# Performance work log

Hardware: AMD Instinct MI355X
Metric: run time of the kernel (lower is better)

Reference implementation:

```python
import jax, jax.numpy as jnp
import numpy as np

IN_DIM = 256
QK_DIM = IN_DIM // 8


def setup_inputs() -> dict:
    key = jax.random.key(0)
    ks = jax.random.split(key, 10)
    B, C, W, H = 4, IN_DIM, 64, 64
    a = jax.random.normal(ks[0], (B, C, W, H), dtype=jnp.float32)
    b = jax.random.normal(ks[1], (B, C, W, H), dtype=jnp.float32)
    c = jax.random.uniform(ks[2], (B, 1, 2 * W, 2 * H), dtype=jnp.float32)
    scale = 0.02
    wq = jax.random.normal(ks[3], (QK_DIM, C), dtype=jnp.float32) * scale
    bq = jnp.zeros((QK_DIM,), dtype=jnp.float32)
    wk = jax.random.normal(ks[4], (QK_DIM, C), dtype=jnp.float32) * scale
    bk = jnp.zeros((QK_DIM,), dtype=jnp.float32)
    wv = jax.random.normal(ks[5], (C, C), dtype=jnp.float32) * scale
    bv = jnp.zeros((C,), dtype=jnp.float32)
    gamma = jnp.ones((1,), dtype=jnp.float32)
    return {"a": a, "b": b, "c": c, "wq": wq, "bq": bq, "wk": wk,
            "bk": bk, "wv": wv, "bv": bv, "gamma": gamma}


def reference(a, b, c, wq, bq, wk, bk, wv, bv, gamma):
    B, C, W, H = a.shape
    N = W * H
    # F.interpolate(c, scale_factor=1/down_rate, mode='nearest'): output idx i -> input idx i*down_rate
    down = c.shape[2] // W
    cd = c[:, :, ::down, ::down]                      # [B,1,W,H]
    # 1x1 convs as channel contractions
    q = jnp.einsum('bchw,oc->bohw', a, wq) + bq[None, :, None, None]
    k = jnp.einsum('bchw,oc->bohw', b, wk) + bk[None, :, None, None]
    v = jnp.einsum('bchw,oc->bohw', a, wv) + bv[None, :, None, None]
    qf = q.reshape(B, QK_DIM, N)                      # proj_query^T rows are spatial
    kf = k.reshape(B, QK_DIM, N)
    vf = v.reshape(B, C, N)
    sim = jnp.einsum('bdi,bdj->bij', qf, kf)          # [B,N,N]
    cflat = cd.reshape(B, N)
    # mask[b,i,j] = cflat[b,i] (per-query multiplicative logit scaling)
    logits = sim * cflat[:, :, None]
    attn = jax.nn.softmax(logits, axis=-1)            # [B,N,N]
    out_attn = jnp.einsum('bcj,bij->bci', vf, attn).reshape(B, C, W, H)
    out = gamma * a * cd + (1.0 - cd) * out_attn
    return out
```

## Files before the change

### kernel.cpp

```cpp
#include <hip/hip_runtime.h>

#define LOG2E 1.44269504088896340736f

typedef __attribute__((ext_vector_type(8))) short short8;
typedef __attribute__((ext_vector_type(4))) float float4v;
typedef __attribute__((ext_vector_type(2))) float float2v;
typedef __attribute__((ext_vector_type(2))) int int2v;
typedef __attribute__((ext_vector_type(4))) int int4v;

__device__ inline unsigned short f2bf(float f) {
    union { float f; unsigned u; } v; v.f = f;
    unsigned r = v.u + 0x7fffu + ((v.u >> 16) & 1u);
    return (unsigned short)(r >> 16);
}
__device__ inline float bf2f(unsigned short u) {
    union { unsigned u; float f; } v; v.u = ((unsigned)u) << 16;
    return v.f;
}
__device__ inline unsigned pk_bf16(float a, float b) {
    union { float f; unsigned u; } ua, ub; ua.f = a; ub.f = b;
    return __builtin_amdgcn_perm(ub.u + 0x8000u, ua.u + 0x8000u, 0x07060302u);
}
__device__ inline unsigned cvtpk_bf16(float a, float b) {
    unsigned r;
    asm("v_cvt_pk_bf16_f32 %0, %1, %2" : "=v"(r) : "v"(a), "v"(b));
    return r;
}

__global__ void wcvt_kernel(const float* __restrict__ wq, const float* __restrict__ wk,
                            const float* __restrict__ wv, unsigned short* __restrict__ Wbf)
{
    int idx = blockIdx.x * 256 + threadIdx.x;
    int e4  = idx * 4;
    int row = e4 >> 8, col = e4 & 255;
    const float* src = (row < 32) ? (wq + row * 256 + col)
                     : (row < 64) ? (wk + (row - 32) * 256 + col)
                                  : (wv + (row - 64) * 256 + col);
    float4v v = *(const float4v*)src;
    int2v p;
    p.x = (unsigned)f2bf(v[0]) | ((unsigned)f2bf(v[1]) << 16);
    p.y = (unsigned)f2bf(v[2]) | ((unsigned)f2bf(v[3]) << 16);
    *(int2v*)(Wbf + e4) = p;
}

__launch_bounds__(512, 2)
__global__ void proj_kernel(const float* __restrict__ a_p, const float* __restrict__ b_p,
                            const float* __restrict__ c_p,
                            const float* __restrict__ bq, const float* __restrict__ bk,
                            const float* __restrict__ bv,
                            const unsigned short* __restrict__ Wbf,
                            unsigned short* __restrict__ Qg, unsigned short* __restrict__ Kg,
                            unsigned short* __restrict__ Vg)
{
    __shared__ __align__(16) unsigned short At[64 * 266];
    __shared__ __align__(16) unsigned short Bt[64 * 266];
    __shared__ float bias[320];
    __shared__ float cdl[64];

    const int t    = threadIdx.x;
    const int blk  = blockIdx.x;
    const int b    = blk & 3;
    const int tile = blk >> 2;
    const int i0   = tile * 64;
    const int lane = t & 63;
    const int w    = t >> 6;
    const int q    = lane >> 4;
    const int n    = lane & 15;
    const int it   = w & 3;
    const int mh   = w >> 2;

    {
        const int arr = t >> 8, tt = t & 255;
        unsigned* dst = (unsigned*)(arr ? Bt : At);
        const float* base = (arr ? b_p : a_p) + (size_t)b * 256 * 4096 + i0;
#pragma unroll
        for (int r = 0; r < 8; ++r) {
            int task = r * 256 + tt;
            int cp = task >> 4, px4 = (task & 15) * 4;
            const float* s0 = base + (size_t)(2 * cp) * 4096 + px4;
            float4v r0 = *(const float4v*)s0;
            float4v r1 = *(const float4v*)(s0 + 4096);
#pragma unroll
            for (int k = 0; k < 4; ++k)
                dst[(px4 + k) * 133 + cp] = pk_bf16(r0[k], r1[k]);
        }
        if (t < 320) bias[t] = (t < 32) ? bq[t] : (t < 64) ? bk[t - 32] : bv[t - 64];
        else if (t < 384) cdl[t - 320] = c_p[b * 16384 + tile * 256 + (t - 320) * 2];
    }
    __syncthreads();

    float4v acc[10];
#pragma unroll
    for (int j = 0; j < 10; ++j) acc[j] = (float4v){0.f, 0.f, 0.f, 0.f};

#pragma unroll 2
    for (int kc = 0; kc < 8; ++kc) {
        short8 xa = *(const short8*)&At[(it * 16 + n) * 266 + kc * 32 + q * 8];
        short8 xb = xa;
        if (mh == 0)
            xb = *(const short8*)&Bt[(it * 16 + n) * 266 + kc * 32 + q * 8];
#pragma unroll
        for (int j = 0; j < 10; ++j) {
            int mt = mh * 10 + j;
            short8 wf = *(const short8*)(Wbf + (size_t)(mt * 16 + n) * 256 + kc * 32 + q * 8);
            short8 bsel = (mt == 2 || mt == 3) ? xb : xa;
            acc[j] = __builtin_amdgcn_mfma_f32_16x16x32_bf16(wf, bsel, acc[j], 0, 0, 0);
        }
    }
    __syncthreads();

    unsigned short* QKst = At;
    unsigned short* Vst  = Bt;
    {
        const float cdq = cdl[it * 16 + n] * LOG2E;
#pragma unroll
        for (int j = 0; j < 10; ++j) {
            int mt = mh * 10 + j;
            float4v bv4 = *(const float4v*)&bias[mt * 16 + q * 4];
            float v0 = acc[j][0] + bv4[0], v1 = acc[j][1] + bv4[1];
            float v2 = acc[j][2] + bv4[2], v3 = acc[j][3] + bv4[3];
            if (mt < 2) {
                v0 *= cdq; v1 *= cdq; v2 *= cdq; v3 *= cdq;
                int2v pk; pk.x = (int)pk_bf16(v0, v1); pk.y = (int)pk_bf16(v2, v3);
                *(int2v*)&QKst[(it * 16 + n) * 72 + mt * 16 + q * 4] = pk;
            } else if (mt < 4) {
                int2v pk; pk.x = (int)pk_bf16(v0, v1); pk.y = (int)pk_bf16(v2, v3);
                *(int2v*)&QKst[(it * 16 + n) * 72 + mt * 16 + q * 4] = pk;
            } else {
                int p = ((n >> 2) * 8) + ((it & 1) * 4) + (n & 3);
                int cbase = mt * 16 - 64 + q * 4;
                int jb = it >> 1;
                Vst[((jb * 256) + cbase + 0) * 32 + p] = f2bf(v0);
                Vst[((jb * 256) + cbase + 1) * 32 + p] = f2bf(v1);
                Vst[((jb * 256) + cbase + 2) * 32 + p] = f2bf(v2);
                Vst[((jb * 256) + cbase + 3) * 32 + p] = f2bf(v3);
            }
        }
    }
    __syncthreads();

    {
        int i = t >> 3, h8 = t & 7;
        int4v v = *(const int4v*)&QKst[i * 72 + h8 * 8];
        unsigned short* dstp = (h8 < 4)
            ? Qg + (size_t)(b * 4096 + i0 + i) * 32 + h8 * 8
            : Kg + (size_t)(b * 4096 + i0 + i) * 32 + (h8 - 4) * 8;
        *(int4v*)dstp = v;
    }
    {
#pragma unroll
        for (int k = 0; k < 4; ++k) {
            int flat = k * 512 + t;
            int4v v = *(const int4v*)&Vst[flat * 8];
            int jb = flat >> 10;
            *(int4v*)(Vg + (size_t)(b * 128 + tile * 2 + jb) * 8192 + (flat & 1023) * 8) = v;
        }
    }
}

__launch_bounds__(256, 3)
__global__ void attn_kernel(const unsigned short* __restrict__ Qg,
                            const unsigned short* __restrict__ Kg,
                            const unsigned short* __restrict__ Vg,
                            unsigned short* __restrict__ Opart, float* __restrict__ lsum)
{
    __shared__ __align__(16) unsigned short Pbuf[2][4][64 * 8];

    const int t    = threadIdx.x;
    const int blk  = blockIdx.x;
    const int b    = blk & 3;
    const int rt   = (blk >> 2) & 63;
    const int s    = blk >> 8;
    const int ni   = (s == 2) ? 32 : 48;
    const int lidx = (s << 8) | (rt << 2) | b;
    const int i0   = rt * 64;
    const int lane = t & 63;
    const int w    = t >> 6;
    const int q    = lane >> 4;
    const int n    = lane & 15;

    short8 qf = *(const short8*)(Qg + (size_t)(b * 4096 + i0 + w * 16 + n) * 32 + q * 8);

    float4v acc[4][4];
#pragma unroll
    for (int ig = 0; ig < 4; ++ig)
#pragma unroll
        for (int ct = 0; ct < 4; ++ct) acc[ig][ct] = (float4v){0.f, 0.f, 0.f, 0.f};
    float lsc = 0.f;

    const float4v m16v = (float4v){-16.f, -16.f, -16.f, -16.f};

    const unsigned short* kb = Kg + (size_t)(b * 4096 + s * 1536 + n) * 32 + q * 8;
    const unsigned short* vb = Vg + ((size_t)((b * 128 + s * 48) * 256 + w * 64 + n)) * 32 + q * 8;

    short8 vf[4];
#pragma unroll
    for (int ct = 0; ct < 4; ++ct)
        vf[ct] = *(const short8*)(vb + ct * 512);
    short8 kf0 = *(const short8*)(kb);
    short8 kf1 = *(const short8*)(kb + 512);

    {
        float4v s0 = __builtin_amdgcn_mfma_f32_16x16x32_bf16(kf0, qf, m16v, 0, 0, 0);
        float4v s1 = __builtin_amdgcn_mfma_f32_16x16x32_bf16(kf1, qf, m16v, 0, 0, 0);
        kf0 = *(const short8*)(kb + 1024);
        kf1 = *(const short8*)(kb + 1536);
        float p0 = __builtin_amdgcn_exp2f(s0[0]), p1 = __builtin_amdgcn_exp2f(s0[1]);
        float p2 = __builtin_amdgcn_exp2f(s0[2]), p3 = __builtin_amdgcn_exp2f(s0[3]);
        float p4 = __builtin_amdgcn_exp2f(s1[0]), p5 = __builtin_amdgcn_exp2f(s1[1]);
        float p6 = __builtin_amdgcn_exp2f(s1[2]), p7 = __builtin_amdgcn_exp2f(s1[3]);
        lsc += ((p0 + p1) + (p2 + p3)) + ((p4 + p5) + (p6 + p7));
        union { short8 s8; unsigned u[4]; } pf_;
        pf_.u[0] = cvtpk_bf16(p0, p1);
        pf_.u[1] = cvtpk_bf16(p2, p3);
        pf_.u[2] = cvtpk_bf16(p4, p5);
        pf_.u[3] = cvtpk_bf16(p6, p7);
        *(short8*)&Pbuf[0][w][lane * 8] = pf_.s8;
    }
    __syncthreads();
    short8 pfc[4];
#pragma unroll
    for (int ig = 0; ig < 4; ++ig)
        pfc[ig] = *(const short8*)&Pbuf[0][ig][lane * 8];

    kb += 2048;
    vb += 8192;

#pragma unroll 1
    for (int it = 0; it < ni - 1; ++it) {
        float4v s0 = __builtin_amdgcn_mfma_f32_16x16x32_bf16(kf0, qf, m16v, 0, 0, 0);
        float4v s1 = __builtin_amdgcn_mfma_f32_16x16x32_bf16(kf1, qf, m16v, 0, 0, 0);
        kf0 = *(const short8*)(kb);
        kf1 = *(const short8*)(kb + 512);

        __builtin_amdgcn_s_setprio(1);
#pragma unroll
        for (int ig = 0; ig < 4; ++ig)
#pragma unroll
            for (int ct = 0; ct < 4; ++ct)
                acc[ig][ct] = __builtin_amdgcn_mfma_f32_16x16x32_bf16(pfc[ig], vf[ct], acc[ig][ct], 0, 0, 0);
        __builtin_amdgcn_s_setprio(0);

#pragma unroll
        for (int ct = 0; ct < 4; ++ct)
            vf[ct] = *(const short8*)(vb + ct * 512);

        {
            float p0 = __builtin_amdgcn_exp2f(s0[0]), p1 = __builtin_amdgcn_exp2f(s0[1]);
            float p2 = __builtin_amdgcn_exp2f(s0[2]), p3 = __builtin_amdgcn_exp2f(s0[3]);
            float p4 = __builtin_amdgcn_exp2f(s1[0]), p5 = __builtin_amdgcn_exp2f(s1[1]);
            float p6 = __builtin_amdgcn_exp2f(s1[2]), p7 = __builtin_amdgcn_exp2f(s1[3]);
            lsc += ((p0 + p1) + (p2 + p3)) + ((p4 + p5) + (p6 + p7));
            union { short8 s8; unsigned u[4]; } pf_;
            pf_.u[0] = cvtpk_bf16(p0, p1);
            pf_.u[1] = cvtpk_bf16(p2, p3);
            pf_.u[2] = cvtpk_bf16(p4, p5);
            pf_.u[3] = cvtpk_bf16(p6, p7);
            *(short8*)&Pbuf[(it + 1) & 1][w][lane * 8] = pf_.s8;
        }
        __syncthreads();
#pragma unroll
        for (int ig = 0; ig < 4; ++ig)
            pfc[ig] = *(const short8*)&Pbuf[(it + 1) & 1][ig][lane * 8];

        kb += 1024;
        vb += 8192;
    }

#pragma unroll
    for (int ig = 0; ig < 4; ++ig)
#pragma unroll
        for (int ct = 0; ct < 4; ++ct)
            acc[ig][ct] = __builtin_amdgcn_mfma_f32_16x16x32_bf16(pfc[ig], vf[ct], acc[ig][ct], 0, 0, 0);

    const size_t obase = (size_t)lidx * 16384;
#pragma unroll
    for (int ig = 0; ig < 4; ++ig)
#pragma unroll
        for (int ct = 0; ct < 4; ++ct) {
            int c = w * 64 + ct * 16 + n;
            int i = ig * 16 + q * 4;
            int2v pk;
            pk.x = (int)pk_bf16(acc[ig][ct][0], acc[ig][ct][1]);
            pk.y = (int)pk_bf16(acc[ig][ct][2], acc[ig][ct][3]);
            *(int2v*)(Opart + obase + (size_t)c * 64 + i) = pk;
        }
    {
        float v = lsc;
        v += __shfl_xor(v, 16, 64);
        v += __shfl_xor(v, 32, 64);
        if (lane < 16)
            lsum[(size_t)lidx * 64 + w * 16 + lane] = v;
    }
}

__launch_bounds__(256, 4)
__global__ void combine_kernel(const float* __restrict__ a_p, const float* __restrict__ c_p,
                               const float* __restrict__ gamma_p,
                               const unsigned short* __restrict__ Opart,
                               const float* __restrict__ lsum, float* __restrict__ out)
{
    __shared__ float invL[64];
    __shared__ float cdl[64];

    const int t   = threadIdx.x;
    const int blk = blockIdx.x;
    const int b   = blk & 3;
    const int rt  = (blk >> 2) & 63;
    const int cs  = blk >> 8;
    const int i0  = rt * 64;

    if (t < 64) {
        float L = 0.f;
#pragma unroll
        for (int s = 0; s < 3; ++s)
            L += lsum[(size_t)((s << 8) | (rt << 2) | b) * 64 + t];
        invL[t] = 1.0f / L;
        cdl[t] = c_p[b * 16384 + rt * 256 + 2 * t];
    }
    __syncthreads();

    const float gam = gamma_p[0];
    const int c  = cs * 32 + (t >> 3);
    const int e8 = (t & 7) * 8;
    float o[8];
#pragma unroll
    for (int r = 0; r < 8; ++r) o[r] = 0.f;
#pragma unroll
    for (int s = 0; s < 3; ++s) {
        int idx = (s << 8) | (rt << 2) | b;
        int4v pv = *(const int4v*)(Opart + (size_t)idx * 16384 + (size_t)c * 64 + e8);
#pragma unroll
        for (int h = 0; h < 4; ++h) {
            unsigned u = (unsigned)pv[h];
            o[2 * h]     += bf2f((unsigned short)(u & 0xffffu));
            o[2 * h + 1] += bf2f((unsigned short)(u >> 16));
        }
    }
    size_t gi = (size_t)(b * 256 + c) * 4096 + i0 + e8;
    float4v a0 = *(const float4v*)(a_p + gi);
    float4v a1 = *(const float4v*)(a_p + gi + 4);
    float4v ov0, ov1;
#pragma unroll
    for (int r = 0; r < 4; ++r) {
        float cd0 = cdl[e8 + r],     l0 = invL[e8 + r];
        float cd1 = cdl[e8 + 4 + r], l1 = invL[e8 + 4 + r];
        ov0[r] = gam * a0[r] * cd0 + (1.0f - cd0) * (o[r] * l0);
        ov1[r] = gam * a1[r] * cd1 + (1.0f - cd1) * (o[4 + r] * l1);
    }
    *(float4v*)(out + gi) = ov0;
    *(float4v*)(out + gi + 4) = ov1;
}

extern "C" void kernel_launch(void* const* d_in, const int* in_sizes, int n_in,
                              void* d_out, int out_size, void* d_ws, size_t ws_size,
                              hipStream_t stream)
{
    const float* a_p   = (const float*)d_in[0];
    const float* b_p   = (const float*)d_in[1];
    const float* c_p   = (const float*)d_in[2];
    const float* wq    = (const float*)d_in[3];
    const float* bq    = (const float*)d_in[4];
    const float* wk    = (const float*)d_in[5];
    const float* bk    = (const float*)d_in[6];
    const float* wv    = (const float*)d_in[7];
    const float* bv    = (const float*)d_in[8];
    const float* gamma = (const float*)d_in[9];
    float* out = (float*)d_out;

    unsigned short* Qg    = (unsigned short*)d_ws;
    unsigned short* Kg    = Qg + (size_t)4 * 4096 * 32;
    unsigned short* Vg    = Kg + (size_t)4 * 4096 * 32;
    unsigned short* Wbf   = Vg + (size_t)4 * 256 * 4096;
    unsigned short* Opart = Wbf + (size_t)320 * 256;
    float*          lsum  = (float*)(Opart + (size_t)768 * 16384);

    wcvt_kernel<<<80, 256, 0, stream>>>(wq, wk, wv, Wbf);
    proj_kernel<<<256, 512, 0, stream>>>(a_p, b_p, c_p, bq, bk, bv, Wbf, Qg, Kg, Vg);
    attn_kernel<<<768, 256, 0, stream>>>(Qg, Kg, Vg, Opart, lsum);
    combine_kernel<<<2048, 256, 0, stream>>>(a_p, c_p, gamma, Opart, lsum, out);
}
```

Baseline: 175.3 us.

## Keep P in registers per wave and split V columns instead of sharing via LDS

Each wave now keeps its own 16 query rows' P fragment in registers and accumulates across all 256 value channels, instead of exchanging P tiles through a double-buffered LDS array with a __syncthreads every iteration. This removes the per-iteration block barrier and LDS traffic. In exchange each wave loads all 16 V fragments per step, four times the V global/L2 read traffic, with register ping-pong prefetching between two V buffers.

Measured after the change: 263.2 us. 1.5x slower.

```diff
diff --git a/kernel.cpp b/kernel.cpp
--- a/kernel.cpp
+++ b/kernel.cpp
@@ -164,8 +164,6 @@
                             const unsigned short* __restrict__ Vg,
                             unsigned short* __restrict__ Opart, float* __restrict__ lsum)
 {
-    __shared__ __align__(16) unsigned short Pbuf[2][4][64 * 8];
-
     const int t    = threadIdx.x;
     const int blk  = blockIdx.x;
     const int b    = blk & 3;
@@ -181,25 +179,20 @@
 
     short8 qf = *(const short8*)(Qg + (size_t)(b * 4096 + i0 + w * 16 + n) * 32 + q * 8);
 
-    float4v acc[4][4];
-#pragma unroll
-    for (int ig = 0; ig < 4; ++ig)
-#pragma unroll
-        for (int ct = 0; ct < 4; ++ct) acc[ig][ct] = (float4v){0.f, 0.f, 0.f, 0.f};
+    float4v acc[16];
+#pragma unroll
+    for (int ct = 0; ct < 16; ++ct) acc[ct] = (float4v){0.f, 0.f, 0.f, 0.f};
     float lsc = 0.f;
 
     const float4v m16v = (float4v){-16.f, -16.f, -16.f, -16.f};
 
     const unsigned short* kb = Kg + (size_t)(b * 4096 + s * 1536 + n) * 32 + q * 8;
-    const unsigned short* vb = Vg + ((size_t)((b * 128 + s * 48) * 256 + w * 64 + n)) * 32 + q * 8;
-
-    short8 vf[4];
-#pragma unroll
-    for (int ct = 0; ct < 4; ++ct)
-        vf[ct] = *(const short8*)(vb + ct * 512);
+    const unsigned short* vb = Vg + ((size_t)((b * 128 + s * 48) * 256 + n)) * 32 + q * 8;
+
     short8 kf0 = *(const short8*)(kb);
     short8 kf1 = *(const short8*)(kb + 512);
 
+    short8 pfc;
     {
         float4v s0 = __builtin_amdgcn_mfma_f32_16x16x32_bf16(kf0, qf, m16v, 0, 0, 0);
         float4v s1 = __builtin_amdgcn_mfma_f32_16x16x32_bf16(kf1, qf, m16v, 0, 0, 0);
@@ -215,16 +208,13 @@
         pf_.u[1] = cvtpk_bf16(p2, p3);
         pf_.u[2] = cvtpk_bf16(p4, p5);
         pf_.u[3] = cvtpk_bf16(p6, p7);
-        *(short8*)&Pbuf[0][w][lane * 8] = pf_.s8;
-    }
-    __syncthreads();
-    short8 pfc[4];
-#pragma unroll
-    for (int ig = 0; ig < 4; ++ig)
-        pfc[ig] = *(const short8*)&Pbuf[0][ig][lane * 8];
-
+        pfc = pf_.s8;
+    }
+    short8 vfP[4], vfQ[4];
+#pragma unroll
+    for (int k = 0; k < 4; ++k)
+        vfP[k] = *(const short8*)(vb + k * 512);
     kb += 2048;
-    vb += 8192;
 
 #pragma unroll 1
     for (int it = 0; it < ni - 1; ++it) {
@@ -235,15 +225,26 @@
 
         __builtin_amdgcn_s_setprio(1);
 #pragma unroll
-        for (int ig = 0; ig < 4; ++ig)
-#pragma unroll
-            for (int ct = 0; ct < 4; ++ct)
-                acc[ig][ct] = __builtin_amdgcn_mfma_f32_16x16x32_bf16(pfc[ig], vf[ct], acc[ig][ct], 0, 0, 0);
+        for (int k = 0; k < 4; ++k) vfQ[k] = *(const short8*)(vb + (4 + k) * 512);
+#pragma unroll
+        for (int k = 0; k < 4; ++k)
+            acc[k] = __builtin_amdgcn_mfma_f32_16x16x32_bf16(pfc, vfP[k], acc[k], 0, 0, 0);
+#pragma unroll
+        for (int k = 0; k < 4; ++k) vfP[k] = *(const short8*)(vb + (8 + k) * 512);
+#pragma unroll
+        for (int k = 0; k < 4; ++k)
+            acc[4 + k] = __builtin_amdgcn_mfma_f32_16x16x32_bf16(pfc, vfQ[k], acc[4 + k], 0, 0, 0);
+#pragma unroll
+        for (int k = 0; k < 4; ++k) vfQ[k] = *(const short8*)(vb + (12 + k) * 512);
+#pragma unroll
+        for (int k = 0; k < 4; ++k)
+            acc[8 + k] = __builtin_amdgcn_mfma_f32_16x16x32_bf16(pfc, vfP[k], acc[8 + k], 0, 0, 0);
+#pragma unroll
+        for (int k = 0; k < 4; ++k) vfP[k] = *(const short8*)(vb + 8192 + k * 512);
+#pragma unroll
+        for (int k = 0; k < 4; ++k)
+            acc[12 + k] = __builtin_amdgcn_mfma_f32_16x16x32_bf16(pfc, vfQ[k], acc[12 + k], 0, 0, 0);
         __builtin_amdgcn_s_setprio(0);
-
-#pragma unroll
-        for (int ct = 0; ct < 4; ++ct)
-            vf[ct] = *(const short8*)(vb + ct * 512);
 
         {
             float p0 = __builtin_amdgcn_exp2f(s0[0]), p1 = __builtin_amdgcn_exp2f(s0[1]);
@@ -256,35 +257,42 @@
             pf_.u[1] = cvtpk_bf16(p2, p3);
             pf_.u[2] = cvtpk_bf16(p4, p5);
             pf_.u[3] = cvtpk_bf16(p6, p7);
-            *(short8*)&Pbuf[(it + 1) & 1][w][lane * 8] = pf_.s8;
-        }
-        __syncthreads();
-#pragma unroll
-        for (int ig = 0; ig < 4; ++ig)
-            pfc[ig] = *(const short8*)&Pbuf[(it + 1) & 1][ig][lane * 8];
+            pfc = pf_.s8;
+        }
 
         kb += 1024;
         vb += 8192;
     }
 
 #pragma unroll
-    for (int ig = 0; ig < 4; ++ig)
-#pragma unroll
-        for (int ct = 0; ct < 4; ++ct)
-            acc[ig][ct] = __builtin_amdgcn_mfma_f32_16x16x32_bf16(pfc[ig], vf[ct], acc[ig][ct], 0, 0, 0);
+    for (int k = 0; k < 4; ++k) vfQ[k] = *(const short8*)(vb + (4 + k) * 512);
+#pragma unroll
+    for (int k = 0; k < 4; ++k)
+        acc[k] = __builtin_amdgcn_mfma_f32_16x16x32_bf16(pfc, vfP[k], acc[k], 0, 0, 0);
+#pragma unroll
+    for (int k = 0; k < 4; ++k) vfP[k] = *(const short8*)(vb + (8 + k) * 512);
+#pragma unroll
+    for (int k = 0; k < 4; ++k)
+        acc[4 + k] = __builtin_amdgcn_mfma_f32_16x16x32_bf16(pfc, vfQ[k], acc[4 + k], 0, 0, 0);
+#pragma unroll
+    for (int k = 0; k < 4; ++k) vfQ[k] = *(const short8*)(vb + (12 + k) * 512);
+#pragma unroll
+    for (int k = 0; k < 4; ++k)
+        acc[8 + k] = __builtin_amdgcn_mfma_f32_16x16x32_bf16(pfc, vfP[k], acc[8 + k], 0, 0, 0);
+#pragma unroll
+    for (int k = 0; k < 4; ++k)
+        acc[12 + k] = __builtin_amdgcn_mfma_f32_16x16x32_bf16(pfc, vfQ[k], acc[12 + k], 0, 0, 0);
 
     const size_t obase = (size_t)lidx * 16384;
 #pragma unroll
-    for (int ig = 0; ig < 4; ++ig)
-#pragma unroll
-        for (int ct = 0; ct < 4; ++ct) {
-            int c = w * 64 + ct * 16 + n;
-            int i = ig * 16 + q * 4;
-            int2v pk;
-            pk.x = (int)pk_bf16(acc[ig][ct][0], acc[ig][ct][1]);
-            pk.y = (int)pk_bf16(acc[ig][ct][2], acc[ig][ct][3]);
-            *(int2v*)(Opart + obase + (size_t)c * 64 + i) = pk;
-        }
+    for (int ct = 0; ct < 16; ++ct) {
+        int c = ct * 16 + n;
+        int i = w * 16 + q * 4;
+        int2v pk;
+        pk.x = (int)pk_bf16(acc[ct][0], acc[ct][1]);
+        pk.y = (int)pk_bf16(acc[ct][2], acc[ct][3]);
+        *(int2v*)(Opart + obase + (size_t)c * 64 + i) = pk;
+    }
     {
         float v = lsc;
         v += __shfl_xor(v, 16, 64);
```

## Process two key tiles per loop iteration to halve barriers in attention

Applied to the files above, without the earlier changes.

Each main-loop iteration now handles two 32-key chunks. It computes four QK MFMAs, writes two P fragments to a doubled LDS buffer, and runs 32 PV MFMAs, so half as many iterations and __syncthreads are needed. V fragments are loaded inside the loop right before use instead of being prefetched one iteration ahead. This trades barrier and loop overhead for higher register pressure and V load latency that is now exposed.

Result: slower. 179.3 us (+2.3%).

```diff
diff --git a/kernel.cpp b/kernel.cpp
--- a/kernel.cpp
+++ b/kernel.cpp
@@ -164,14 +164,14 @@
                             const unsigned short* __restrict__ Vg,
                             unsigned short* __restrict__ Opart, float* __restrict__ lsum)
 {
-    __shared__ __align__(16) unsigned short Pbuf[2][4][64 * 8];
+    __shared__ __align__(16) unsigned short Pbuf[2][4][2][64 * 8];
 
     const int t    = threadIdx.x;
     const int blk  = blockIdx.x;
     const int b    = blk & 3;
     const int rt   = (blk >> 2) & 63;
     const int s    = blk >> 8;
-    const int ni   = (s == 2) ? 32 : 48;
+    const int nr   = (s == 2) ? 16 : 24;
     const int lidx = (s << 8) | (rt << 2) | b;
     const int i0   = rt * 64;
     const int lane = t & 63;
@@ -193,85 +193,127 @@
     const unsigned short* kb = Kg + (size_t)(b * 4096 + s * 1536 + n) * 32 + q * 8;
     const unsigned short* vb = Vg + ((size_t)((b * 128 + s * 48) * 256 + w * 64 + n)) * 32 + q * 8;
 
-    short8 vf[4];
-#pragma unroll
-    for (int ct = 0; ct < 4; ++ct)
-        vf[ct] = *(const short8*)(vb + ct * 512);
-    short8 kf0 = *(const short8*)(kb);
-    short8 kf1 = *(const short8*)(kb + 512);
-
-    {
-        float4v s0 = __builtin_amdgcn_mfma_f32_16x16x32_bf16(kf0, qf, m16v, 0, 0, 0);
-        float4v s1 = __builtin_amdgcn_mfma_f32_16x16x32_bf16(kf1, qf, m16v, 0, 0, 0);
-        kf0 = *(const short8*)(kb + 1024);
-        kf1 = *(const short8*)(kb + 1536);
-        float p0 = __builtin_amdgcn_exp2f(s0[0]), p1 = __builtin_amdgcn_exp2f(s0[1]);
-        float p2 = __builtin_amdgcn_exp2f(s0[2]), p3 = __builtin_amdgcn_exp2f(s0[3]);
-        float p4 = __builtin_amdgcn_exp2f(s1[0]), p5 = __builtin_amdgcn_exp2f(s1[1]);
-        float p6 = __builtin_amdgcn_exp2f(s1[2]), p7 = __builtin_amdgcn_exp2f(s1[3]);
-        lsc += ((p0 + p1) + (p2 + p3)) + ((p4 + p5) + (p6 + p7));
-        union { short8 s8; unsigned u[4]; } pf_;
-        pf_.u[0] = cvtpk_bf16(p0, p1);
-        pf_.u[1] = cvtpk_bf16(p2, p3);
-        pf_.u[2] = cvtpk_bf16(p4, p5);
-        pf_.u[3] = cvtpk_bf16(p6, p7);
-        *(short8*)&Pbuf[0][w][lane * 8] = pf_.s8;
+    short8 kfs[4];
+#pragma unroll
+    for (int k = 0; k < 4; ++k) kfs[k] = *(const short8*)(kb + k * 512);
+
+    {
+        float4v sA0 = __builtin_amdgcn_mfma_f32_16x16x32_bf16(kfs[0], qf, m16v, 0, 0, 0);
+        float4v sA1 = __builtin_amdgcn_mfma_f32_16x16x32_bf16(kfs[1], qf, m16v, 0, 0, 0);
+        float4v sB0 = __builtin_amdgcn_mfma_f32_16x16x32_bf16(kfs[2], qf, m16v, 0, 0, 0);
+        float4v sB1 = __builtin_amdgcn_mfma_f32_16x16x32_bf16(kfs[3], qf, m16v, 0, 0, 0);
+#pragma unroll
+        for (int k = 0; k < 4; ++k) kfs[k] = *(const short8*)(kb + 2048 + k * 512);
+        float a0 = __builtin_amdgcn_exp2f(sA0[0]), a1 = __builtin_amdgcn_exp2f(sA0[1]);
+        float a2 = __builtin_amdgcn_exp2f(sA0[2]), a3 = __builtin_amdgcn_exp2f(sA0[3]);
+        float a4 = __builtin_amdgcn_exp2f(sA1[0]), a5 = __builtin_amdgcn_exp2f(sA1[1]);
+        float a6 = __builtin_amdgcn_exp2f(sA1[2]), a7 = __builtin_amdgcn_exp2f(sA1[3]);
+        float b0 = __builtin_amdgcn_exp2f(sB0[0]), b1 = __builtin_amdgcn_exp2f(sB0[1]);
+        float b2 = __builtin_amdgcn_exp2f(sB0[2]), b3 = __builtin_amdgcn_exp2f(sB0[3]);
+        float b4 = __builtin_amdgcn_exp2f(sB1[0]), b5 = __builtin_amdgcn_exp2f(sB1[1]);
+        float b6 = __builtin_amdgcn_exp2f(sB1[2]), b7 = __builtin_amdgcn_exp2f(sB1[3]);
+        lsc += ((a0 + a1) + (a2 + a3)) + ((a4 + a5) + (a6 + a7))
+             + ((b0 + b1) + (b2 + b3)) + ((b4 + b5) + (b6 + b7));
+        union { short8 s8; unsigned u[4]; } pA_, pB_;
+        pA_.u[0] = cvtpk_bf16(a0, a1); pA_.u[1] = cvtpk_bf16(a2, a3);
+        pA_.u[2] = cvtpk_bf16(a4, a5); pA_.u[3] = cvtpk_bf16(a6, a7);
+        pB_.u[0] = cvtpk_bf16(b0, b1); pB_.u[1] = cvtpk_bf16(b2, b3);
+        pB_.u[2] = cvtpk_bf16(b4, b5); pB_.u[3] = cvtpk_bf16(b6, b7);
+        *(short8*)&Pbuf[0][w][0][lane * 8] = pA_.s8;
+        *(short8*)&Pbuf[0][w][1][lane * 8] = pB_.s8;
     }
     __syncthreads();
-    short8 pfc[4];
-#pragma unroll
-    for (int ig = 0; ig < 4; ++ig)
-        pfc[ig] = *(const short8*)&Pbuf[0][ig][lane * 8];
-
-    kb += 2048;
-    vb += 8192;
+    short8 pfc[4][2];
+#pragma unroll
+    for (int ig = 0; ig < 4; ++ig) {
+        pfc[ig][0] = *(const short8*)&Pbuf[0][ig][0][lane * 8];
+        pfc[ig][1] = *(const short8*)&Pbuf[0][ig][1][lane * 8];
+    }
+    kb += 4096;
 
 #pragma unroll 1
-    for (int it = 0; it < ni - 1; ++it) {
-        float4v s0 = __builtin_amdgcn_mfma_f32_16x16x32_bf16(kf0, qf, m16v, 0, 0, 0);
-        float4v s1 = __builtin_amdgcn_mfma_f32_16x16x32_bf16(kf1, qf, m16v, 0, 0, 0);
-        kf0 = *(const short8*)(kb);
-        kf1 = *(const short8*)(kb + 512);
+    for (int r = 0; r < nr - 1; ++r) {
+        float4v sA0 = __builtin_amdgcn_mfma_f32_16x16x32_bf16(kfs[0], qf, m16v, 0, 0, 0);
+        float4v sA1 = __builtin_amdgcn_mfma_f32_16x16x32_bf16(kfs[1], qf, m16v, 0, 0, 0);
+        float4v sB0 = __builtin_amdgcn_mfma_f32_16x16x32_bf16(kfs[2], qf, m16v, 0, 0, 0);
+        float4v sB1 = __builtin_amdgcn_mfma_f32_16x16x32_bf16(kfs[3], qf, m16v, 0, 0, 0);
+#pragma unroll
+        for (int k = 0; k < 4; ++k) kfs[k] = *(const short8*)(kb + k * 512);
 
         __builtin_amdgcn_s_setprio(1);
-#pragma unroll
-        for (int ig = 0; ig < 4; ++ig)
+        {
+            short8 vf[4];
 #pragma unroll
             for (int ct = 0; ct < 4; ++ct)
-                acc[ig][ct] = __builtin_amdgcn_mfma_f32_16x16x32_bf16(pfc[ig], vf[ct], acc[ig][ct], 0, 0, 0);
+                vf[ct] = *(const short8*)(vb + ct * 512);
+#pragma unroll
+            for (int ig = 0; ig < 4; ++ig)
+#pragma unroll
+                for (int ct = 0; ct < 4; ++ct)
+                    acc[ig][ct] = __builtin_amdgcn_mfma_f32_16x16x32_bf16(pfc[ig][0], vf[ct], acc[ig][ct], 0, 0, 0);
+        }
+        {
+            short8 vf[4];
+#pragma unroll
+            for (int ct = 0; ct < 4; ++ct)
+                vf[ct] = *(const short8*)(vb + 8192 + ct * 512);
+#pragma unroll
+            for (int ig = 0; ig < 4; ++ig)
+#pragma unroll
+                for (int ct = 0; ct < 4; ++ct)
+                    acc[ig][ct] = __builtin_amdgcn_mfma_f32_16x16x32_bf16(pfc[ig][1], vf[ct], acc[ig][ct], 0, 0, 0);
+        }
         __builtin_amdgcn_s_setprio(0);
 
+        {
+            float a0 = __builtin_amdgcn_exp2f(sA0[0]), a1 = __builtin_amdgcn_exp2f(sA0[1]);
+            float a2 = __builtin_amdgcn_exp2f(sA0[2]), a3 = __builtin_amdgcn_exp2f(sA0[3]);
+            float a4 = __builtin_amdgcn_exp2f(sA1[0]), a5 = __builtin_amdgcn_exp2f(sA1[1]);
+            float a6 = __builtin_amdgcn_exp2f(sA1[2]), a7 = __builtin_amdgcn_exp2f(sA1[3]);
+            float b0 = __builtin_amdgcn_exp2f(sB0[0]), b1 = __builtin_amdgcn_exp2f(sB0[1]);
+            float b2 = __builtin_amdgcn_exp2f(sB0[2]), b3 = __builtin_amdgcn_exp2f(sB0[3]);
+            float b4 = __builtin_amdgcn_exp2f(sB1[0]), b5 = __builtin_amdgcn_exp2f(sB1[1]);
+            float b6 = __builtin_amdgcn_exp2f(sB1[2]), b7 = __builtin_amdgcn_exp2f(sB1[3]);
+            lsc += ((a0 + a1) + (a2 + a3)) + ((a4 + a5) + (a6 + a7))
+                 + ((b0 + b1) + (b2 + b3)) + ((b4 + b5) + (b6 + b7));
+            union { short8 s8; unsigned u[4]; } pA_, pB_;
+            pA_.u[0] = cvtpk_bf16(a0, a1); pA_.u[1] = cvtpk_bf16(a2, a3);
+            pA_.u[2] = cvtpk_bf16(a4, a5); pA_.u[3] = cvtpk_bf16(a6, a7);
+            pB_.u[0] = cvtpk_bf16(b0, b1); pB_.u[1] = cvtpk_bf16(b2, b3);
+            pB_.u[2] = cvtpk_bf16(b4, b5); pB_.u[3] = cvtpk_bf16(b6, b7);
+            *(short8*)&Pbuf[(r + 1) & 1][w][0][lane * 8] = pA_.s8;
+            *(short8*)&Pbuf[(r + 1) & 1][w][1][lane * 8] = pB_.s8;
+        }
+        __syncthreads();
+#pragma unroll
+        for (int ig = 0; ig < 4; ++ig) {
+            pfc[ig][0] = *(const short8*)&Pbuf[(r + 1) & 1][ig][0][lane * 8];
+            pfc[ig][1] = *(const short8*)&Pbuf[(r + 1) & 1][ig][1][lane * 8];
+        }
+
+        kb += 2048;
+        vb += 16384;
+    }
+
+    {
+        short8 vf[4];
 #pragma unroll
         for (int ct = 0; ct < 4; ++ct)
             vf[ct] = *(const short8*)(vb + ct * 512);
-
-        {
-            float p0 = __builtin_amdgcn_exp2f(s0[0]), p1 = __builtin_amdgcn_exp2f(s0[1]);
-            float p2 = __builtin_amdgcn_exp2f(s0[2]), p3 = __builtin_amdgcn_exp2f(s0[3]);
-            float p4 = __builtin_amdgcn_exp2f(s1[0]), p5 = __builtin_amdgcn_exp2f(s1[1]);
-            float p6 = __builtin_amdgcn_exp2f(s1[2]), p7 = __builtin_amdgcn_exp2f(s1[3]);
-            lsc += ((p0 + p1) + (p2 + p3)) + ((p4 + p5) + (p6 + p7));
-            union { short8 s8; unsigned u[4]; } pf_;
-            pf_.u[0] = cvtpk_bf16(p0, p1);
-            pf_.u[1] = cvtpk_bf16(p2, p3);
-            pf_.u[2] = cvtpk_bf16(p4, p5);
-            pf_.u[3] = cvtpk_bf16(p6, p7);
-            *(short8*)&Pbuf[(it + 1) & 1][w][lane * 8] = pf_.s8;
-        }
-        __syncthreads();
 #pragma unroll
         for (int ig = 0; ig < 4; ++ig)
-            pfc[ig] = *(const short8*)&Pbuf[(it + 1) & 1][ig][lane * 8];
-
-        kb += 1024;
-        vb += 8192;
-    }
-
-#pragma unroll
-    for (int ig = 0; ig < 4; ++ig)
+#pragma unroll
+            for (int ct = 0; ct < 4; ++ct)
+                acc[ig][ct] = __builtin_amdgcn_mfma_f32_16x16x32_bf16(pfc[ig][0], vf[ct], acc[ig][ct], 0, 0, 0);
 #pragma unroll
         for (int ct = 0; ct < 4; ++ct)
-            acc[ig][ct] = __builtin_amdgcn_mfma_f32_16x16x32_bf16(pfc[ig], vf[ct], acc[ig][ct], 0, 0, 0);
+            vf[ct] = *(const short8*)(vb + 8192 + ct * 512);
+#pragma unroll
+        for (int ig = 0; ig < 4; ++ig)
+#pragma unroll
+            for (int ct = 0; ct < 4; ++ct)
+                acc[ig][ct] = __builtin_amdgcn_mfma_f32_16x16x32_bf16(pfc[ig][1], vf[ct], acc[ig][ct], 0, 0, 0);
+    }
 
     const size_t obase = (size_t)lidx * 16384;
 #pragma unroll
```
